# Performance work log

Measured on AMD Instinct MI355X. Metric: run time of the kernel, lower is better.

The kernel has to match this reference:

```python
import jax, jax.numpy as jnp
import numpy as np

B, S, D, U = 64, 2048, 512, 512

def setup_inputs() -> dict:
    key = jax.random.key(0)
    ks = jax.random.split(key, 8)
    query = jax.random.normal(ks[0], (B, D), dtype=jnp.float32)
    values = jax.random.normal(ks[1], (B, S, D), dtype=jnp.float32)
    # Keras Dense params (glorot-like scale), with biases (Dense default use_bias=True)
    W1 = jax.random.normal(ks[2], (D, U), dtype=jnp.float32) / np.sqrt(D)
    b1 = jnp.zeros((U,), dtype=jnp.float32)
    W2 = jax.random.normal(ks[3], (D, U), dtype=jnp.float32) / np.sqrt(D)
    b2 = jnp.zeros((U,), dtype=jnp.float32)
    V = jax.random.normal(ks[4], (U, 1), dtype=jnp.float32) / np.sqrt(U)
    bv = jnp.zeros((1,), dtype=jnp.float32)
    return {"query": query, "values": values, "W1": W1, "b1": b1,
            "W2": W2, "b2": b2, "V": V, "bv": bv}

def reference(query, values, W1, b1, W2, b2, V, bv) -> jnp.ndarray:
    # query: [B, D], values: [B, S, D]
    q_proj = query @ W1 + b1                      # [B, U]
    v_proj = jnp.einsum('bsd,du->bsu', values, W2) + b2  # [B, S, U]
    h = jnp.tanh(q_proj[:, None, :] + v_proj)     # [B, S, U]
    scores = jnp.einsum('bsu,uo->bso', h, V) + bv # [B, S, 1]
    attn = jax.nn.softmax(scores, axis=1)         # softmax over sequence axis
    context = jnp.sum(attn * values, axis=1)      # [B, D]
    return context
```

## Files before the change

kernel.cpp:

```cpp
#include <hip/hip_runtime.h>
#include <hip/hip_bf16.h>

#define BB 64
#define SS 2048
#define DD 512
#define UU 512
#define BS (BB*SS)

typedef __attribute__((ext_vector_type(8))) short bf16x8;
typedef __attribute__((ext_vector_type(16))) float f32x16;

static __device__ __forceinline__ unsigned short f2bf(float x) {
    union { float f; unsigned int u; } v; v.f = x;
    unsigned int r = v.u + 0x7FFFu + ((v.u >> 16) & 1u);
    return (unsigned short)(r >> 16);
}

__global__ void k_prep(const float* __restrict__ W2, unsigned short* __restrict__ W2F,
                       const float* __restrict__ query, const float* __restrict__ W1,
                       const float* __restrict__ b1, const float* __restrict__ b2,
                       float* __restrict__ qpb) {
    __shared__ float tile[64][65];
    __shared__ float qs[512];
    const int t = threadIdx.x;
    if (blockIdx.x < 64) {
        const int ti = blockIdx.x >> 3;
        const int tj = blockIdx.x & 7;
        #pragma unroll
        for (int i = 0; i < 16; ++i) {
            int e = i*256 + t;
            int dr = e >> 6, uc = e & 63;
            tile[dr][uc] = W2[(size_t)(ti*64+dr)*UU + tj*64+uc];
        }
        __syncthreads();
        const int ksl = t >> 6, ln = t & 63;
        const int lh = ln >> 5, l31 = ln & 31;
        #pragma unroll
        for (int ntl = 0; ntl < 2; ++ntl) {
            const int ks = ti*4 + ksl;
            const int ntile = tj*2 + ntl;
            bf16x8 g;
            #pragma unroll
            for (int j = 0; j < 8; ++j)
                g[j] = (short)f2bf(tile[ksl*16 + lh*8 + j][ntl*32 + l31]);
            *(bf16x8*)&W2F[(size_t)(((ks*16 + ntile)*64 + ln) * 8)] = g;
        }
    } else {
        const int idx = blockIdx.x - 64;
        const int b  = idx >> 1;
        const int uh = idx & 1;
        const int u  = uh*256 + t;
        if (t < 256) { qs[t] = query[b*DD + t]; qs[t+256] = query[b*DD + t + 256]; }
        __syncthreads();
        float p0 = 0.f, p1 = 0.f, p2 = 0.f, p3 = 0.f;
        #pragma unroll 2
        for (int d = 0; d < DD; d += 4) {
            p0 = fmaf(qs[d+0], W1[(size_t)(d+0)*UU + u], p0);
            p1 = fmaf(qs[d+1], W1[(size_t)(d+1)*UU + u], p1);
            p2 = fmaf(qs[d+2], W1[(size_t)(d+2)*UU + u], p2);
            p3 = fmaf(qs[d+3], W1[(size_t)(d+3)*UU + u], p3);
        }
        qpb[b*UU + u] = (p0 + p1) + (p2 + p3) + b1[u] + b2[u];
    }
}

__launch_bounds__(512, 4)
__global__ void k_scores(const float* __restrict__ values,
                         const unsigned short* __restrict__ W2F,
                         const float* __restrict__ qpb,
                         const float* __restrict__ Vw,
                         float* __restrict__ pm, float* __restrict__ pl,
                         float* __restrict__ pv) {
    __shared__ unsigned short Albuf[64*512];
    const int t   = threadIdx.x;
    const int blk = blockIdx.x;
    const int m0  = blk * 64;
    const int b   = blk >> 5;
    const int wave = t >> 6, lane = t & 63;
    const int ln31 = lane & 31, half = lane >> 5;

    const bf16x8* Bp = (const bf16x8*)W2F;
    bf16x8 bfr[2][2];
    #pragma unroll
    for (int nt = 0; nt < 2; ++nt)
        bfr[0][nt] = Bp[(0*16 + wave*2 + nt)*64 + lane];
    #pragma unroll
    for (int nt = 0; nt < 2; ++nt)
        bfr[1][nt] = Bp[(1*16 + wave*2 + nt)*64 + lane];

    float qv[2], vw[2];
    #pragma unroll
    for (int nt = 0; nt < 2; ++nt) {
        int n = wave*64 + nt*32 + ln31;
        qv[nt] = qpb[b*UU + n];
        vw[nt] = Vw[n];
    }

    const float* src = values + (size_t)m0 * DD;
    #pragma unroll
    for (int i = 0; i < 8; ++i) {
        int gf  = i*512 + t;
        int row = gf >> 6;
        int g   = gf & 63;
        const float4 f0 = *(const float4*)(src + (size_t)row*DD + g*8);
        const float4 f1 = *(const float4*)(src + (size_t)row*DD + g*8 + 4);
        bf16x8 pk;
        pk[0] = (short)f2bf(f0.x); pk[1] = (short)f2bf(f0.y);
        pk[2] = (short)f2bf(f0.z); pk[3] = (short)f2bf(f0.w);
        pk[4] = (short)f2bf(f1.x); pk[5] = (short)f2bf(f1.y);
        pk[6] = (short)f2bf(f1.z); pk[7] = (short)f2bf(f1.w);
        *(bf16x8*)&Albuf[row*512 + ((g ^ (row & 7)) << 3)] = pk;
    }
    __syncthreads();

    f32x16 acc[2][2];
    #pragma unroll
    for (int mt = 0; mt < 2; ++mt)
        #pragma unroll
        for (int nt = 0; nt < 2; ++nt)
            #pragma unroll
            for (int r = 0; r < 16; ++r)
                acc[mt][nt][r] = 0.f;

    const int xm = ln31 & 7;
    #pragma unroll 4
    for (int ks = 0; ks < 32; ++ks) {
        const int cur = ks & 1;
        const int g8 = (((ks*2 + half) ^ xm) << 3);
        bf16x8 a0 = *(const bf16x8*)&Albuf[ln31*512 + g8];
        bf16x8 a1 = *(const bf16x8*)&Albuf[16384 + ln31*512 + g8];
        #pragma unroll
        for (int nt = 0; nt < 2; ++nt) {
            acc[0][nt] = __builtin_amdgcn_mfma_f32_32x32x16_bf16(a0, bfr[cur][nt], acc[0][nt], 0, 0, 0);
            acc[1][nt] = __builtin_amdgcn_mfma_f32_32x32x16_bf16(a1, bfr[cur][nt], acc[1][nt], 0, 0, 0);
        }
        #pragma unroll
        for (int nt = 0; nt < 2; ++nt)
            bfr[cur][nt] = Bp[((ks+2)*16 + wave*2 + nt)*64 + lane];
    }

    __syncthreads();
    float* sred = (float*)Albuf;

    #pragma unroll
    for (int mt = 0; mt < 2; ++mt) {
        float s[16];
        #pragma unroll
        for (int r = 0; r < 16; ++r) s[r] = 0.f;
        #pragma unroll
        for (int nt = 0; nt < 2; ++nt) {
            const float q = qv[nt], w = vw[nt];
            #pragma unroll
            for (int r = 0; r < 16; ++r) {
                float x = q + acc[mt][nt][r];
                float e = __expf(x + x);
                float rc = __builtin_amdgcn_rcpf(e + 1.f);
                s[r] = fmaf(fmaf(-2.f, rc, 1.f), w, s[r]);
            }
        }
        #pragma unroll
        for (int r = 0; r < 16; ++r) {
            float v = s[r];
            v += __shfl_xor(v, 1);
            v += __shfl_xor(v, 2);
            v += __shfl_xor(v, 4);
            v += __shfl_xor(v, 8);
            v += __shfl_xor(v, 16);
            if (ln31 == 0)
                sred[wave*64 + mt*32 + (r & 3) + 8*(r >> 2) + 4*half] = v;
        }
    }
    __syncthreads();

    if (t < 64) {
        float s = 0.f;
        #pragma unroll
        for (int w = 0; w < 8; ++w) s += sred[w*64 + t];
        float m = s;
        #pragma unroll
        for (int off = 32; off; off >>= 1) m = fmaxf(m, __shfl_xor(m, off));
        float p = __expf(s - m);
        float l = p;
        #pragma unroll
        for (int off = 32; off; off >>= 1) l += __shfl_xor(l, off);
        sred[512 + t] = p;
        if (t == 0) { pm[blk] = m; pl[blk] = l; }
    }
    __syncthreads();

    const int tt = t & 255, th = t >> 8;
    const float* sp = sred + 512;
    float2 cacc = make_float2(0.f, 0.f);
    const float* vrow = values + (size_t)m0*DD + tt*2;
    #pragma unroll 8
    for (int i = 0; i < 32; ++i) {
        const int rowi = th*32 + i;
        float p = sp[rowi];
        float2 v = *(const float2*)(vrow + (size_t)rowi*DD);
        cacc.x = fmaf(p, v.x, cacc.x);
        cacc.y = fmaf(p, v.y, cacc.y);
    }
    float2* cred = (float2*)(sred + 576);
    if (th == 1) cred[tt] = cacc;
    __syncthreads();
    if (th == 0) {
        float2 o = cred[tt];
        cacc.x += o.x; cacc.y += o.y;
        *(float2*)&pv[(size_t)blk*DD + tt*2] = cacc;
    }
}

__global__ void k_finish(const float* __restrict__ pv, const float* __restrict__ pm,
                         const float* __restrict__ pl, float* __restrict__ out) {
    __shared__ float sm_[32], sl_[32], sw[32];
    const int b = blockIdx.x, t = threadIdx.x;
    if (t < 32) { sm_[t] = pm[b*32 + t]; sl_[t] = pl[b*32 + t]; }
    __syncthreads();
    float M = -1e30f;
    #pragma unroll
    for (int c = 0; c < 32; ++c) M = fmaxf(M, sm_[c]);
    float L = 0.f;
    #pragma unroll
    for (int c = 0; c < 32; ++c) L += sl_[c] * __expf(sm_[c] - M);
    if (t < 32) sw[t] = __expf(sm_[t] - M) / L;
    __syncthreads();
    float2 a = make_float2(0.f, 0.f);
    #pragma unroll 4
    for (int c = 0; c < 32; ++c) {
        float w = sw[c];
        float2 v = *(const float2*)&pv[(size_t)(b*32 + c)*DD + t*2];
        a.x = fmaf(w, v.x, a.x);
        a.y = fmaf(w, v.y, a.y);
    }
    *(float2*)&out[(size_t)b*DD + t*2] = a;
}

extern "C" void kernel_launch(void* const* d_in, const int* in_sizes, int n_in,
                              void* d_out, int out_size, void* d_ws, size_t ws_size,
                              hipStream_t stream) {
    const float* query  = (const float*)d_in[0];
    const float* values = (const float*)d_in[1];
    const float* W1     = (const float*)d_in[2];
    const float* b1     = (const float*)d_in[3];
    const float* W2     = (const float*)d_in[4];
    const float* b2     = (const float*)d_in[5];
    const float* Vw     = (const float*)d_in[6];

    char* ws = (char*)d_ws;
    unsigned short* W2F = (unsigned short*)ws;
    float* qpb = (float*)(ws + 557056);
    float* pm  = (float*)(ws + 557056 + 131072);
    float* pl  = (float*)(ws + 557056 + 131072 + 8192);
    float* pv  = (float*)(ws + 557056 + 131072 + 16384);

    k_prep<<<192, 256, 0, stream>>>(W2, W2F, query, W1, b1, b2, qpb);
    k_scores<<<BS/64, 512, 0, stream>>>(values, W2F, qpb, Vw, pm, pl, pv);
    k_finish<<<BB, 256, 0, stream>>>(pv, pm, pl, (float*)d_out);
}
```

Before: 499.5 us.

## Make scores kernel persistent with double-buffered LDS prefetch of value tiles

Converts k_scores from one block per 64-row tile into 256 persistent blocks that each process 8 consecutive tiles. The next tile's fp32 values are loaded into registers, converted to bf16 and written to a second LDS buffer, interleaved with the MFMA loop on the current tile. This is meant to hide global load latency behind compute. It also widens the W2 fragment prefetch ring to 4 slots, changes the swizzle, and has every wave compute the softmax partials redundantly, with each thread doing one column of the weighted sum. Occupancy drops (launch bounds 2, 64KB+ of LDS), and only 256 blocks means fewer waves in flight to cover latency.

```diff
diff --git a/kernel.cpp b/kernel.cpp
--- a/kernel.cpp
+++ b/kernel.cpp
@@ -64,29 +64,30 @@
     }
 }
 
-__launch_bounds__(512, 4)
+__launch_bounds__(512, 2)
 __global__ void k_scores(const float* __restrict__ values,
                          const unsigned short* __restrict__ W2F,
                          const float* __restrict__ qpb,
                          const float* __restrict__ Vw,
                          float* __restrict__ pm, float* __restrict__ pl,
                          float* __restrict__ pv) {
-    __shared__ unsigned short Albuf[64*512];
-    const int t   = threadIdx.x;
-    const int blk = blockIdx.x;
-    const int m0  = blk * 64;
-    const int b   = blk >> 5;
+    __shared__ unsigned short Albuf[2][64*512];
+    __shared__ float sred[512];
+    const int t    = threadIdx.x;
+    const int blk  = blockIdx.x;
     const int wave = t >> 6, lane = t & 63;
     const int ln31 = lane & 31, half = lane >> 5;
+    const int b    = blk >> 2;
+    const int srow = t >> 6;
+    const int sg   = t & 63;
 
     const bf16x8* Bp = (const bf16x8*)W2F;
-    bf16x8 bfr[2][2];
-    #pragma unroll
-    for (int nt = 0; nt < 2; ++nt)
-        bfr[0][nt] = Bp[(0*16 + wave*2 + nt)*64 + lane];
-    #pragma unroll
-    for (int nt = 0; nt < 2; ++nt)
-        bfr[1][nt] = Bp[(1*16 + wave*2 + nt)*64 + lane];
+    bf16x8 bfr[4][2];
+    #pragma unroll
+    for (int s = 0; s < 4; ++s)
+        #pragma unroll
+        for (int nt = 0; nt < 2; ++nt)
+            bfr[s][nt] = Bp[(s*16 + wave*2 + nt)*64 + lane];
 
     float qv[2], vw[2];
     #pragma unroll
@@ -96,117 +97,141 @@
         vw[nt] = Vw[n];
     }
 
-    const float* src = values + (size_t)m0 * DD;
-    #pragma unroll
+    {
+        const float* src0 = values + (size_t)blk * 8 * 64 * DD;
+        #pragma unroll
+        for (int c = 0; c < 8; ++c) {
+            const int row = c*8 + srow;
+            const float4 f0 = *(const float4*)(src0 + (size_t)row*DD + sg*8);
+            const float4 f1 = *(const float4*)(src0 + (size_t)row*DD + sg*8 + 4);
+            bf16x8 pk;
+            pk[0] = (short)f2bf(f0.x); pk[1] = (short)f2bf(f0.y);
+            pk[2] = (short)f2bf(f0.z); pk[3] = (short)f2bf(f0.w);
+            pk[4] = (short)f2bf(f1.x); pk[5] = (short)f2bf(f1.y);
+            pk[6] = (short)f2bf(f1.z); pk[7] = (short)f2bf(f1.w);
+            *(bf16x8*)&Albuf[0][row*512 + ((sg ^ (row & 31)) << 3)] = pk;
+        }
+    }
+    asm volatile("s_waitcnt lgkmcnt(0)" ::: "memory");
+    __builtin_amdgcn_s_barrier();
+
+    int cur = 0;
     for (int i = 0; i < 8; ++i) {
-        int gf  = i*512 + t;
-        int row = gf >> 6;
-        int g   = gf & 63;
-        const float4 f0 = *(const float4*)(src + (size_t)row*DD + g*8);
-        const float4 f1 = *(const float4*)(src + (size_t)row*DD + g*8 + 4);
-        bf16x8 pk;
-        pk[0] = (short)f2bf(f0.x); pk[1] = (short)f2bf(f0.y);
-        pk[2] = (short)f2bf(f0.z); pk[3] = (short)f2bf(f0.w);
-        pk[4] = (short)f2bf(f1.x); pk[5] = (short)f2bf(f1.y);
-        pk[6] = (short)f2bf(f1.z); pk[7] = (short)f2bf(f1.w);
-        *(bf16x8*)&Albuf[row*512 + ((g ^ (row & 7)) << 3)] = pk;
-    }
-    __syncthreads();
-
-    f32x16 acc[2][2];
-    #pragma unroll
-    for (int mt = 0; mt < 2; ++mt)
-        #pragma unroll
-        for (int nt = 0; nt < 2; ++nt)
-            #pragma unroll
-            for (int r = 0; r < 16; ++r)
-                acc[mt][nt][r] = 0.f;
-
-    const int xm = ln31 & 7;
-    #pragma unroll 4
-    for (int ks = 0; ks < 32; ++ks) {
-        const int cur = ks & 1;
-        const int g8 = (((ks*2 + half) ^ xm) << 3);
-        bf16x8 a0 = *(const bf16x8*)&Albuf[ln31*512 + g8];
-        bf16x8 a1 = *(const bf16x8*)&Albuf[16384 + ln31*512 + g8];
-        #pragma unroll
-        for (int nt = 0; nt < 2; ++nt) {
-            acc[0][nt] = __builtin_amdgcn_mfma_f32_32x32x16_bf16(a0, bfr[cur][nt], acc[0][nt], 0, 0, 0);
-            acc[1][nt] = __builtin_amdgcn_mfma_f32_32x32x16_bf16(a1, bfr[cur][nt], acc[1][nt], 0, 0, 0);
-        }
-        #pragma unroll
-        for (int nt = 0; nt < 2; ++nt)
-            bfr[cur][nt] = Bp[((ks+2)*16 + wave*2 + nt)*64 + lane];
-    }
-
-    __syncthreads();
-    float* sred = (float*)Albuf;
-
-    #pragma unroll
-    for (int mt = 0; mt < 2; ++mt) {
-        float s[16];
-        #pragma unroll
-        for (int r = 0; r < 16; ++r) s[r] = 0.f;
-        #pragma unroll
-        for (int nt = 0; nt < 2; ++nt) {
-            const float q = qv[nt], w = vw[nt];
+        const int tile = blk*8 + i;
+        const size_t m0 = (size_t)tile * 64;
+        const unsigned short* Ab = Albuf[cur];
+        unsigned short* An = Albuf[cur ^ 1];
+        const float* nsrc = values + (m0 + 64) * DD;
+        const bool st = (i < 7);
+
+        float4 sreg[16];
+        auto issue2 = [&](int c) {
+            const int row = c*8 + srow;
+            sreg[2*c]   = *(const float4*)(nsrc + (size_t)row*DD + sg*8);
+            sreg[2*c+1] = *(const float4*)(nsrc + (size_t)row*DD + sg*8 + 4);
+        };
+        auto flush2 = [&](int c) {
+            const int row = c*8 + srow;
+            bf16x8 pk;
+            pk[0] = (short)f2bf(sreg[2*c].x);   pk[1] = (short)f2bf(sreg[2*c].y);
+            pk[2] = (short)f2bf(sreg[2*c].z);   pk[3] = (short)f2bf(sreg[2*c].w);
+            pk[4] = (short)f2bf(sreg[2*c+1].x); pk[5] = (short)f2bf(sreg[2*c+1].y);
+            pk[6] = (short)f2bf(sreg[2*c+1].z); pk[7] = (short)f2bf(sreg[2*c+1].w);
+            *(bf16x8*)&An[row*512 + ((sg ^ (row & 31)) << 3)] = pk;
+        };
+
+        if (st) { issue2(0); issue2(1); issue2(2); issue2(3); }
+
+        f32x16 acc[2][2];
+        #pragma unroll
+        for (int mt = 0; mt < 2; ++mt)
+            #pragma unroll
+            for (int nt = 0; nt < 2; ++nt)
+                #pragma unroll
+                for (int r = 0; r < 16; ++r)
+                    acc[mt][nt][r] = 0.f;
+
+        #pragma unroll
+        for (int grp = 0; grp < 4; ++grp) {
+            #pragma unroll
+            for (int k8 = 0; k8 < 8; ++k8) {
+                const int ks = grp*8 + k8;
+                const int slot = ks & 3;
+                const int g8 = (((ks*2 + half) ^ ln31) << 3);
+                bf16x8 a0 = *(const bf16x8*)&Ab[ln31*512 + g8];
+                bf16x8 a1 = *(const bf16x8*)&Ab[16384 + ln31*512 + g8];
+                acc[0][0] = __builtin_amdgcn_mfma_f32_32x32x16_bf16(a0, bfr[slot][0], acc[0][0], 0, 0, 0);
+                acc[1][0] = __builtin_amdgcn_mfma_f32_32x32x16_bf16(a1, bfr[slot][0], acc[1][0], 0, 0, 0);
+                acc[0][1] = __builtin_amdgcn_mfma_f32_32x32x16_bf16(a0, bfr[slot][1], acc[0][1], 0, 0, 0);
+                acc[1][1] = __builtin_amdgcn_mfma_f32_32x32x16_bf16(a1, bfr[slot][1], acc[1][1], 0, 0, 0);
+                const int nk = (ks + 4) & 31;
+                bfr[slot][0] = Bp[(nk*16 + wave*2 + 0)*64 + lane];
+                bfr[slot][1] = Bp[(nk*16 + wave*2 + 1)*64 + lane];
+            }
+            if (st) {
+                if (grp == 0)      { flush2(0); flush2(1); issue2(4); issue2(5); }
+                else if (grp == 1) { flush2(2); flush2(3); issue2(6); issue2(7); }
+                else if (grp == 2) { flush2(4); flush2(5); }
+                else               { flush2(6); flush2(7); }
+            }
+        }
+
+        asm volatile("s_waitcnt lgkmcnt(0)" ::: "memory");
+        __builtin_amdgcn_s_barrier();
+
+        #pragma unroll
+        for (int mt = 0; mt < 2; ++mt) {
+            float s[16];
+            #pragma unroll
+            for (int r = 0; r < 16; ++r) s[r] = 0.f;
+            #pragma unroll
+            for (int nt = 0; nt < 2; ++nt) {
+                const float q = qv[nt], w = vw[nt];
+                #pragma unroll
+                for (int r = 0; r < 16; ++r) {
+                    float x = q + acc[mt][nt][r];
+                    float e = __expf(x + x);
+                    float rc = __builtin_amdgcn_rcpf(e + 1.f);
+                    s[r] = fmaf(fmaf(-2.f, rc, 1.f), w, s[r]);
+                }
+            }
             #pragma unroll
             for (int r = 0; r < 16; ++r) {
-                float x = q + acc[mt][nt][r];
-                float e = __expf(x + x);
-                float rc = __builtin_amdgcn_rcpf(e + 1.f);
-                s[r] = fmaf(fmaf(-2.f, rc, 1.f), w, s[r]);
-            }
-        }
-        #pragma unroll
-        for (int r = 0; r < 16; ++r) {
-            float v = s[r];
-            v += __shfl_xor(v, 1);
-            v += __shfl_xor(v, 2);
-            v += __shfl_xor(v, 4);
-            v += __shfl_xor(v, 8);
-            v += __shfl_xor(v, 16);
-            if (ln31 == 0)
-                sred[wave*64 + mt*32 + (r & 3) + 8*(r >> 2) + 4*half] = v;
-        }
-    }
-    __syncthreads();
-
-    if (t < 64) {
-        float s = 0.f;
-        #pragma unroll
-        for (int w = 0; w < 8; ++w) s += sred[w*64 + t];
-        float m = s;
-        #pragma unroll
-        for (int off = 32; off; off >>= 1) m = fmaxf(m, __shfl_xor(m, off));
-        float p = __expf(s - m);
+                float v = s[r];
+                v += __shfl_xor(v, 1);
+                v += __shfl_xor(v, 2);
+                v += __shfl_xor(v, 4);
+                v += __shfl_xor(v, 8);
+                v += __shfl_xor(v, 16);
+                if (ln31 == 0)
+                    sred[wave*64 + mt*32 + (r & 3) + 8*(r >> 2) + 4*half] = v;
+            }
+        }
+        asm volatile("s_waitcnt lgkmcnt(0)" ::: "memory");
+        __builtin_amdgcn_s_barrier();
+
+        float ssum = 0.f;
+        #pragma unroll
+        for (int w = 0; w < 8; ++w) ssum += sred[w*64 + lane];
+        float mx = ssum;
+        #pragma unroll
+        for (int off = 32; off; off >>= 1) mx = fmaxf(mx, __shfl_xor(mx, off));
+        float p = __expf(ssum - mx);
         float l = p;
         #pragma unroll
         for (int off = 32; off; off >>= 1) l += __shfl_xor(l, off);
-        sred[512 + t] = p;
-        if (t == 0) { pm[blk] = m; pl[blk] = l; }
-    }
-    __syncthreads();
-
-    const int tt = t & 255, th = t >> 8;
-    const float* sp = sred + 512;
-    float2 cacc = make_float2(0.f, 0.f);
-    const float* vrow = values + (size_t)m0*DD + tt*2;
-    #pragma unroll 8
-    for (int i = 0; i < 32; ++i) {
-        const int rowi = th*32 + i;
-        float p = sp[rowi];
-        float2 v = *(const float2*)(vrow + (size_t)rowi*DD);
-        cacc.x = fmaf(p, v.x, cacc.x);
-        cacc.y = fmaf(p, v.y, cacc.y);
-    }
-    float2* cred = (float2*)(sred + 576);
-    if (th == 1) cred[tt] = cacc;
-    __syncthreads();
-    if (th == 0) {
-        float2 o = cred[tt];
-        cacc.x += o.x; cacc.y += o.y;
-        *(float2*)&pv[(size_t)blk*DD + tt*2] = cacc;
+        if (t == 0) { pm[tile] = mx; pl[tile] = l; }
+
+        float ca = 0.f;
+        const float* vcol = values + m0*DD + t;
+        #pragma unroll 8
+        for (int r = 0; r < 64; ++r) {
+            float pr = __shfl(p, r);
+            ca = fmaf(pr, vcol[(size_t)r*DD], ca);
+        }
+        pv[(size_t)tile*DD + t] = ca;
+
+        cur ^= 1;
     }
 }
 
@@ -254,6 +279,6 @@
     float* pv  = (float*)(ws + 557056 + 131072 + 16384);
 
     k_prep<<<192, 256, 0, stream>>>(W2, W2F, query, W1, b1, b2, qpb);
-    k_scores<<<BS/64, 512, 0, stream>>>(values, W2F, qpb, Vw, pm, pl, pv);
+    k_scores<<<256, 512, 0, stream>>>(values, W2F, qpb, Vw, pm, pl, pv);
     k_finish<<<BB, 256, 0, stream>>>(pv, pm, pl, (float*)d_out);
 }
```

Result: slower. 843.6 us (+68.9%).

## Deepen B-fragment prefetch, widen LDS swizzle, and make every wave do the softmax

Applied to the files above, without the earlier changes.

The W2 fragment register prefetch goes from two stages to four, the LDS XOR swizzle widens from 8 to 32 groups, and the MFMA cluster is bracketed with s_setprio. __syncthreads is replaced with an explicit lgkmcnt wait plus s_barrier. The single-wave softmax and two-half context reduction are replaced by every wave computing the softmax redundantly and broadcasting probabilities through shuffles, so each thread accumulates one column over all 64 rows with no extra barriers. This trades more registers and redundant exp work for fewer synchronisations and less LDS traffic. The workspace offsets also change, which may signal a larger W2F layout in the hidden prep kernel.

```diff
diff --git a/kernel.cpp b/kernel.cpp
--- a/kernel.cpp
+++ b/kernel.cpp
@@ -80,13 +80,12 @@
     const int ln31 = lane & 31, half = lane >> 5;
 
     const bf16x8* Bp = (const bf16x8*)W2F;
-    bf16x8 bfr[2][2];
-    #pragma unroll
-    for (int nt = 0; nt < 2; ++nt)
-        bfr[0][nt] = Bp[(0*16 + wave*2 + nt)*64 + lane];
-    #pragma unroll
-    for (int nt = 0; nt < 2; ++nt)
-        bfr[1][nt] = Bp[(1*16 + wave*2 + nt)*64 + lane];
+    bf16x8 bfr[4][2];
+    #pragma unroll
+    for (int s = 0; s < 4; ++s)
+        #pragma unroll
+        for (int nt = 0; nt < 2; ++nt)
+            bfr[s][nt] = Bp[(s*16 + wave*2 + nt)*64 + lane];
 
     float qv[2], vw[2];
     #pragma unroll
@@ -109,9 +108,10 @@
         pk[2] = (short)f2bf(f0.z); pk[3] = (short)f2bf(f0.w);
         pk[4] = (short)f2bf(f1.x); pk[5] = (short)f2bf(f1.y);
         pk[6] = (short)f2bf(f1.z); pk[7] = (short)f2bf(f1.w);
-        *(bf16x8*)&Albuf[row*512 + ((g ^ (row & 7)) << 3)] = pk;
-    }
-    __syncthreads();
+        *(bf16x8*)&Albuf[row*512 + ((g ^ (row & 31)) << 3)] = pk;
+    }
+    asm volatile("s_waitcnt lgkmcnt(0)" ::: "memory");
+    __builtin_amdgcn_s_barrier();
 
     f32x16 acc[2][2];
     #pragma unroll
@@ -122,24 +122,24 @@
             for (int r = 0; r < 16; ++r)
                 acc[mt][nt][r] = 0.f;
 
-    const int xm = ln31 & 7;
     #pragma unroll 4
     for (int ks = 0; ks < 32; ++ks) {
-        const int cur = ks & 1;
-        const int g8 = (((ks*2 + half) ^ xm) << 3);
+        const int slot = ks & 3;
+        const int g8 = (((ks*2 + half) ^ ln31) << 3);
         bf16x8 a0 = *(const bf16x8*)&Albuf[ln31*512 + g8];
         bf16x8 a1 = *(const bf16x8*)&Albuf[16384 + ln31*512 + g8];
-        #pragma unroll
-        for (int nt = 0; nt < 2; ++nt) {
-            acc[0][nt] = __builtin_amdgcn_mfma_f32_32x32x16_bf16(a0, bfr[cur][nt], acc[0][nt], 0, 0, 0);
-            acc[1][nt] = __builtin_amdgcn_mfma_f32_32x32x16_bf16(a1, bfr[cur][nt], acc[1][nt], 0, 0, 0);
-        }
-        #pragma unroll
-        for (int nt = 0; nt < 2; ++nt)
-            bfr[cur][nt] = Bp[((ks+2)*16 + wave*2 + nt)*64 + lane];
-    }
-
-    __syncthreads();
+        __builtin_amdgcn_s_setprio(1);
+        acc[0][0] = __builtin_amdgcn_mfma_f32_32x32x16_bf16(a0, bfr[slot][0], acc[0][0], 0, 0, 0);
+        acc[1][0] = __builtin_amdgcn_mfma_f32_32x32x16_bf16(a1, bfr[slot][0], acc[1][0], 0, 0, 0);
+        acc[0][1] = __builtin_amdgcn_mfma_f32_32x32x16_bf16(a0, bfr[slot][1], acc[0][1], 0, 0, 0);
+        acc[1][1] = __builtin_amdgcn_mfma_f32_32x32x16_bf16(a1, bfr[slot][1], acc[1][1], 0, 0, 0);
+        __builtin_amdgcn_s_setprio(0);
+        bfr[slot][0] = Bp[((ks+4)*16 + wave*2 + 0)*64 + lane];
+        bfr[slot][1] = Bp[((ks+4)*16 + wave*2 + 1)*64 + lane];
+    }
+
+    asm volatile("s_waitcnt lgkmcnt(0)" ::: "memory");
+    __builtin_amdgcn_s_barrier();
     float* sred = (float*)Albuf;
 
     #pragma unroll
@@ -170,44 +170,29 @@
                 sred[wave*64 + mt*32 + (r & 3) + 8*(r >> 2) + 4*half] = v;
         }
     }
-    __syncthreads();
-
-    if (t < 64) {
-        float s = 0.f;
-        #pragma unroll
-        for (int w = 0; w < 8; ++w) s += sred[w*64 + t];
-        float m = s;
-        #pragma unroll
-        for (int off = 32; off; off >>= 1) m = fmaxf(m, __shfl_xor(m, off));
-        float p = __expf(s - m);
-        float l = p;
-        #pragma unroll
-        for (int off = 32; off; off >>= 1) l += __shfl_xor(l, off);
-        sred[512 + t] = p;
-        if (t == 0) { pm[blk] = m; pl[blk] = l; }
-    }
-    __syncthreads();
-
-    const int tt = t & 255, th = t >> 8;
-    const float* sp = sred + 512;
-    float2 cacc = make_float2(0.f, 0.f);
-    const float* vrow = values + (size_t)m0*DD + tt*2;
+    asm volatile("s_waitcnt lgkmcnt(0)" ::: "memory");
+    __builtin_amdgcn_s_barrier();
+
+    float ssum = 0.f;
+    #pragma unroll
+    for (int w = 0; w < 8; ++w) ssum += sred[w*64 + lane];
+    float mx = ssum;
+    #pragma unroll
+    for (int off = 32; off; off >>= 1) mx = fmaxf(mx, __shfl_xor(mx, off));
+    float p = __expf(ssum - mx);
+    float l = p;
+    #pragma unroll
+    for (int off = 32; off; off >>= 1) l += __shfl_xor(l, off);
+    if (t == 0) { pm[blk] = mx; pl[blk] = l; }
+
+    float ca = 0.f;
+    const float* vcol = values + (size_t)m0*DD + t;
     #pragma unroll 8
-    for (int i = 0; i < 32; ++i) {
-        const int rowi = th*32 + i;
-        float p = sp[rowi];
-        float2 v = *(const float2*)(vrow + (size_t)rowi*DD);
-        cacc.x = fmaf(p, v.x, cacc.x);
-        cacc.y = fmaf(p, v.y, cacc.y);
-    }
-    float2* cred = (float2*)(sred + 576);
-    if (th == 1) cred[tt] = cacc;
-    __syncthreads();
-    if (th == 0) {
-        float2 o = cred[tt];
-        cacc.x += o.x; cacc.y += o.y;
-        *(float2*)&pv[(size_t)blk*DD + tt*2] = cacc;
-    }
+    for (int r = 0; r < 64; ++r) {
+        float pr = __shfl(p, r);
+        ca = fmaf(pr, vcol[(size_t)r*DD], ca);
+    }
+    pv[(size_t)blk*DD + t] = ca;
 }
 
 __global__ void k_finish(const float* __restrict__ pv, const float* __restrict__ pm,
@@ -248,10 +233,10 @@
 
     char* ws = (char*)d_ws;
     unsigned short* W2F = (unsigned short*)ws;
-    float* qpb = (float*)(ws + 557056);
-    float* pm  = (float*)(ws + 557056 + 131072);
-    float* pl  = (float*)(ws + 557056 + 131072 + 8192);
-    float* pv  = (float*)(ws + 557056 + 131072 + 16384);
+    float* qpb = (float*)(ws + 589824);
+    float* pm  = (float*)(ws + 589824 + 131072);
+    float* pl  = (float*)(ws + 589824 + 131072 + 8192);
+    float* pv  = (float*)(ws + 589824 + 131072 + 16384);
 
     k_prep<<<192, 256, 0, stream>>>(W2, W2F, query, W1, b1, b2, qpb);
     k_scores<<<BS/64, 512, 0, stream>>>(values, W2F, qpb, Vw, pm, pl, pv);
```

Measured after the change: 475.3 us. -4.9%, faster.
